# Kernel optimization log

Measured on AMD Instinct MI355X. Metric: run time of the kernel, lower is better.

Reference implementation:

```python
import jax, jax.numpy as jnp
import numpy as np

ALPHA = 0.5        # damping from conf['alpha']
MAX_ITERS = 30     # fixed-point iterations (conf uses up to 150 with eps early-exit)
GN_GROUPS = 3
GN_EPS = 1e-5
SLOPE = 0.01       # F.leaky_relu default negative_slope


def _conv(x, w, b, pad):
    y = jax.lax.conv_general_dilated(
        x, w, window_strides=(1, 1), padding=[(pad, pad), (pad, pad)],
        dimension_numbers=("NCHW", "OIHW", "NCHW"))
    return y + b[None, :, None, None]


def _leaky(x):
    return jnp.where(x >= 0, x, SLOPE * x)


def _groupnorm(x, gamma, beta):
    N, C, H, W = x.shape
    xg = x.reshape(N, GN_GROUPS, C // GN_GROUPS, H, W)
    mu = xg.mean(axis=(2, 3, 4), keepdims=True)
    var = xg.var(axis=(2, 3, 4), keepdims=True)
    xg = (xg - mu) * jax.lax.rsqrt(var + GN_EPS)
    x = xg.reshape(N, C, H, W)
    return x * gamma[None, :, None, None] + beta[None, :, None, None]


def setup_inputs() -> dict:
    key = jax.random.key(0)
    ks = jax.random.split(key, 8)
    image = jax.random.normal(ks[0], (1024, 3, 32, 32), dtype=jnp.float32)
    # Unit params (small init keeps the fixed-point iteration contractive)
    w1 = jax.random.normal(ks[1], (6, 8, 5, 5), dtype=jnp.float32) * 0.05
    b1 = jnp.zeros((6,), jnp.float32)
    gamma = jnp.ones((6,), jnp.float32)
    beta = jnp.zeros((6,), jnp.float32)
    w2 = jax.random.normal(ks[2], (5, 6, 5, 5), dtype=jnp.float32) * 0.05
    b2 = jnp.zeros((5,), jnp.float32)
    # detection head: Conv2d(5, 10, 32, padding=0) -> full-image conv
    wh = jax.random.normal(ks[3], (10, 5, 32, 32), dtype=jnp.float32) * 0.01
    bh = jnp.zeros((10,), jnp.float32)
    return {"image": image, "w1": w1, "b1": b1, "gamma": gamma, "beta": beta,
            "w2": w2, "b2": b2, "wh": wh, "bh": bh}


def reference(image, w1, b1, gamma, beta, w2, b2, wh, bh):
    N = image.shape[0]
    z0 = jnp.zeros((N, 5, 32, 32), image.dtype)

    def unit(z):
        zx = jnp.concatenate([z, image], axis=1)
        h = _groupnorm(_leaky(_conv(zx, w1, b1, 2)), gamma, beta)
        return _leaky(_conv(h, w2, b2, 2))

    def step(z, _):
        z = (1.0 - ALPHA) * z + ALPHA * unit(z)
        return z, None

    z, _ = jax.lax.scan(step, z0, None, length=MAX_ITERS)
    return _conv(z, wh, bh, 0)
```

## Files before the change

### kernel.cpp

```cpp
#include <hip/hip_runtime.h>
#include <hip/hip_fp16.h>


typedef _Float16 half8 __attribute__((ext_vector_type(8)));
typedef float f32x4 __attribute__((ext_vector_type(4)));

#define PLANE 5184
#define HB    5184
#define WL1   10368
#define WL2   12928
#define NLDS  15488

__device__ __forceinline__ unsigned pk2(float a, float b) {
    __half2 h = __float22half2_rn(make_float2(a, b));
    return *reinterpret_cast<unsigned*>(&h);
}
__device__ __forceinline__ float2 up2(unsigned u) {
    __half2 h = *reinterpret_cast<__half2*>(&u);
    return __half22float2(h);
}
__device__ __forceinline__ unsigned hmul2(unsigned a, unsigned b) {
    __half2 r = __hmul2(*reinterpret_cast<__half2*>(&a), *reinterpret_cast<__half2*>(&b));
    return *reinterpret_cast<unsigned*>(&r);
}
__device__ __forceinline__ float lrelu(float x) { return fmaxf(x, 0.01f * x); }
__device__ __forceinline__ int bofs(int y, int x) {
    return ((y * 36 + x) * 16) ^ ((x & 8) << 1);
}

__global__ void pack_weights(const float* __restrict__ w1,
                             const float* __restrict__ w2,
                             unsigned* __restrict__ ws)
{
    int t = blockIdx.x * 256 + threadIdx.x;
    if (t < 640) {
        int c = t >> 6, l = t & 63;
        int row = l & 15, tg = l >> 4;
        int dx = row >> 3, oc = row & 7;
        int ty = c >> 1, tx = 4 * (c & 1) + tg, kx = tx - dx;
        unsigned q[4];
        #pragma unroll
        for (int d = 0; d < 4; ++d) {
            float v0 = 0.f, v1 = 0.f;
            if (oc < 6 && kx >= 0 && kx < 5) {
                v0 = w1[(oc * 8 + 2 * d) * 25 + ty * 5 + kx];
                v1 = w1[(oc * 8 + 2 * d + 1) * 25 + ty * 5 + kx];
            }
            q[d] = pk2(v0, v1);
        }
        *(uint4*)&ws[t * 4] = make_uint4(q[0], q[1], q[2], q[3]);
    } else if (t < 1280) {
        int u = t - 640;
        int c = u >> 6, l = u & 63;
        int row = l & 15, tg = l >> 4;
        int dx = row >> 3, oc = row & 7;
        int ty = c >> 1, tx = 4 * (c & 1) + tg, kx = tx - dx;
        unsigned q[4];
        #pragma unroll
        for (int d = 0; d < 4; ++d) {
            float v0 = 0.f, v1 = 0.f;
            if (oc < 5 && kx >= 0 && kx < 5) {
                if (2 * d < 6)     v0 = w2[(oc * 6 + 2 * d) * 25 + ty * 5 + kx];
                if (2 * d + 1 < 6) v1 = w2[(oc * 6 + 2 * d + 1) * 25 + ty * 5 + kx];
            }
            q[d] = pk2(v0, v1);
        }
        *(uint4*)&ws[2560 + u * 4] = make_uint4(q[0], q[1], q[2], q[3]);
    } else if (t < 1310) {
        int idx = t - 1280;
        int oc = idx / 6, ch = idx % 6;
        float s = 0.f;
        for (int tap = 0; tap < 25; ++tap) s += w2[(oc * 6 + ch) * 25 + tap];
        ((float*)ws)[5120 + idx] = s;
    }
}

__global__ __launch_bounds__(256, 2)
void deq_kernel(const float* __restrict__ image,
                const unsigned* __restrict__ wks,
                const float* __restrict__ b1,
                const float* __restrict__ gam, const float* __restrict__ bet,
                const float* __restrict__ b2,
                const float* __restrict__ wh, const float* __restrict__ bh,
                float* __restrict__ out)
{
    __shared__ __align__(16) unsigned lds[NLDS];
    __shared__ float red[48];
    __shared__ float s2s[32];

    const int n    = blockIdx.x;
    const int tid  = threadIdx.x;
    const int lane = tid & 63;
    const int wid  = tid >> 6;
    const int col  = lane & 15;
    const int tg   = lane >> 4;
    const int dxl  = tg >> 1;
    const int sub  = tg & 1;

    for (int p = tid; p < 2 * PLANE; p += 256) lds[p] = 0u;
    for (int p = tid; p < 2560; p += 256) {
        lds[WL1 + p] = wks[p];
        lds[WL2 + p] = wks[2560 + p];
    }
    if (tid < 30) s2s[tid] = ((const float*)wks)[5120 + tid];
    __syncthreads();

    {
        const int yy = tid >> 3, xx0 = (tid & 7) << 2;
        float4 i0 = *(const float4*)&image[(n * 3 + 0) * 1024 + yy * 32 + xx0];
        float4 i1 = *(const float4*)&image[(n * 3 + 1) * 1024 + yy * 32 + xx0];
        float4 i2 = *(const float4*)&image[(n * 3 + 2) * 1024 + yy * 32 + xx0];
        float a0[4] = {i0.x, i0.y, i0.z, i0.w};
        float a1[4] = {i1.x, i1.y, i1.z, i1.w};
        float a2[4] = {i2.x, i2.y, i2.z, i2.w};
        #pragma unroll
        for (int i = 0; i < 4; ++i) {
            unsigned* bp = (unsigned*)((char*)lds + bofs(yy + 2, xx0 + 2 + i));
            bp[2] = pk2(0.f, a0[i]);
            bp[3] = pk2(a1[i], a2[i]);
        }
    }

    int sx2[2];
    #pragma unroll
    for (int txh = 0; txh < 2; ++txh) {
        int x = 2 * col + 4 * txh + tg;
        sx2[txh] = (x * 16) ^ ((x & 8) << 1);
    }

    float b1q[4], b2q[4];
    #pragma unroll
    for (int r = 0; r < 4; ++r) {
        int oc = (tg * 4 + r) & 7;
        b1q[r] = (oc < 6) ? b1[oc] : 0.f;
        b2q[r] = (oc < 5) ? b2[oc] : 0.f;
    }
    const f32x4 ai1 = {b1q[0], b1q[1], b1q[2], b1q[3]};

    __syncthreads();

    const char* zb  = (const char*)lds;
    const char* hbB = (const char*)lds + HB * 4;
    const int ay0 = wid << 3;
    const int wlo = lane << 2;

    #pragma unroll 1
    for (int it = 0; it < 30; ++it) {
        uint4 f1[10];
        #pragma unroll
        for (int c = 0; c < 10; ++c)
            f1[c] = *(const uint4*)&lds[WL1 + c * 256 + wlo];

        f32x4 acc[8];
        #pragma unroll
        for (int g = 0; g < 8; ++g) acc[g] = ai1;

        #pragma unroll
        for (int pr = 0; pr < 12; ++pr) {
            const char* rowp = zb + (ay0 + pr) * 576;
            #pragma unroll
            for (int txh = 0; txh < 2; ++txh) {
                half8 pv = *(const half8*)(rowp + sx2[txh]);
                #pragma unroll
                for (int ty = 0; ty < 5; ++ty) {
                    const int g = pr - ty;
                    if (g >= 0 && g < 8)
                        acc[g] = __builtin_amdgcn_mfma_f32_16x16x32_f16(
                            __builtin_bit_cast(half8, f1[ty * 2 + txh]), pv, acc[g], 0, 0, 0);
                }
            }
        }

        float ps_lo = 0.f, ps_hi = 0.f, pq_lo = 0.f, pq_hi = 0.f;
        #pragma unroll
        for (int g = 0; g < 8; ++g) {
            float h0 = lrelu(acc[g][0]), h1 = lrelu(acc[g][1]);
            float h2 = lrelu(acc[g][2]), h3 = lrelu(acc[g][3]);
            ps_lo += h0 + h1;  pq_lo = fmaf(h0, h0, fmaf(h1, h1, pq_lo));
            ps_hi += h2 + h3;  pq_hi = fmaf(h2, h2, fmaf(h3, h3, pq_hi));
            char* wp = (char*)lds + HB * 4 + bofs(ay0 + g + 2, 2 * col + dxl + 2) + sub * 8;
            *(uint2*)wp = make_uint2(pk2(h0, h1), pk2(h2, h3));
        }

        #pragma unroll
        for (int m = 1; m <= 8; m <<= 1) {
            ps_lo += __shfl_xor(ps_lo, m); ps_hi += __shfl_xor(ps_hi, m);
            pq_lo += __shfl_xor(pq_lo, m); pq_hi += __shfl_xor(pq_hi, m);
        }
        ps_lo += __shfl_xor(ps_lo, 32); ps_hi += __shfl_xor(ps_hi, 32);
        pq_lo += __shfl_xor(pq_lo, 32); pq_hi += __shfl_xor(pq_hi, 32);
        if (lane == 0)  { red[wid * 8 + 0] = ps_lo; red[wid * 8 + 1] = ps_hi;
                          red[wid * 8 + 4] = pq_lo; red[wid * 8 + 5] = pq_hi; }
        if (lane == 16) { red[wid * 8 + 2] = ps_lo; red[wid * 8 + 6] = pq_lo; }
        __syncthreads();

        float scv[6], shv[6];
        #pragma unroll
        for (int g3 = 0; g3 < 3; ++g3) {
            float s = 0.f, q = 0.f;
            #pragma unroll
            for (int w = 0; w < 4; ++w) { s += red[w * 8 + g3]; q += red[w * 8 + 4 + g3]; }
            float mean = s * (1.f / 2048.f);
            float var  = q * (1.f / 2048.f) - mean * mean;
            float inv  = rsqrtf(var + 1e-5f);
            #pragma unroll
            for (int k = 0; k < 2; ++k) {
                int c = 2 * g3 + k;
                scv[c] = inv * gam[c];
                shv[c] = bet[c] - mean * scv[c];
            }
        }
        f32x4 ai2;
        #pragma unroll
        for (int r = 0; r < 4; ++r) {
            int ocr = (tg * 4 + r) & 7;
            int base = (ocr < 5) ? ocr * 6 : 0;
            float db = 0.f;
            #pragma unroll
            for (int ch = 0; ch < 6; ++ch) db = fmaf(s2s[base + ch], shv[ch], db);
            ai2[r] = b2q[r] + ((ocr < 5) ? db : 0.f);
        }
        unsigned sp0 = pk2(scv[0], scv[1]), sp1 = pk2(scv[2], scv[3]), sp2 = pk2(scv[4], scv[5]);
        {
            float ph[6];
            #pragma unroll
            for (int c = 0; c < 6; ++c) {
                float rs = (fabsf(scv[c]) > 1e-20f) ? 1.f / scv[c] : 0.f;
                ph[c] = -shv[c] * rs;
            }
            uint4 padq = make_uint4(pk2(ph[0], ph[1]), pk2(ph[2], ph[3]), pk2(ph[4], ph[5]), 0u);
            for (int t = tid; t < 272; t += 256) {
                int row, cc;
                if (t < 72)       { row = t / 36;             cc = t % 36; }
                else if (t < 144) { row = 34 + (t - 72) / 36; cc = (t - 72) % 36; }
                else {
                    int q4 = t - 144;
                    row = 2 + (q4 >> 2);
                    int c4 = q4 & 3;
                    cc = (c4 < 2) ? c4 : c4 + 32;
                }
                *(uint4*)((char*)lds + HB * 4 + bofs(row, cc)) = padq;
            }
        }
        __syncthreads();

        uint4 f2[10];
        #pragma unroll
        for (int c = 0; c < 10; ++c) {
            uint4 wr = *(const uint4*)&lds[WL2 + c * 256 + wlo];
            f2[c].x = hmul2(wr.x, sp0);
            f2[c].y = hmul2(wr.y, sp1);
            f2[c].z = hmul2(wr.z, sp2);
            f2[c].w = 0u;
        }
        #pragma unroll
        for (int g = 0; g < 8; ++g) acc[g] = ai2;

        #pragma unroll
        for (int pr = 0; pr < 12; ++pr) {
            const char* rowp = hbB + (ay0 + pr) * 576;
            #pragma unroll
            for (int txh = 0; txh < 2; ++txh) {
                half8 pv = *(const half8*)(rowp + sx2[txh]);
                #pragma unroll
                for (int ty = 0; ty < 5; ++ty) {
                    const int g = pr - ty;
                    if (g >= 0 && g < 8)
                        acc[g] = __builtin_amdgcn_mfma_f32_16x16x32_f16(
                            __builtin_bit_cast(half8, f2[ty * 2 + txh]), pv, acc[g], 0, 0, 0);
                }
            }
        }

        #pragma unroll
        for (int g = 0; g < 8; ++g) {
            char* zp = (char*)lds + bofs(ay0 + g + 2, 2 * col + dxl + 2);
            if (sub == 0) {
                uint2 zo = *(uint2*)zp;
                float2 za = up2(zo.x), zc = up2(zo.y);
                float z0 = 0.5f * za.x + 0.5f * lrelu(acc[g][0]);
                float z1 = 0.5f * za.y + 0.5f * lrelu(acc[g][1]);
                float z2 = 0.5f * zc.x + 0.5f * lrelu(acc[g][2]);
                float z3 = 0.5f * zc.y + 0.5f * lrelu(acc[g][3]);
                *(uint2*)zp = make_uint2(pk2(z0, z1), pk2(z2, z3));
            } else {
                _Float16* pz = (_Float16*)(zp + 8);
                float z4 = 0.5f * (float)pz[0] + 0.5f * lrelu(acc[g][0]);
                pz[0] = (_Float16)z4;
            }
        }
        __syncthreads();
    }

    {
        const int yy = tid >> 3, xx0 = (tid & 7) << 2;
        float zf[5][4];
        #pragma unroll
        for (int i = 0; i < 4; ++i) {
            const unsigned* bp = (const unsigned*)((const char*)lds + bofs(yy + 2, xx0 + 2 + i));
            float2 f0 = up2(bp[0]), f1 = up2(bp[1]), f2 = up2(bp[2]);
            zf[0][i] = f0.x; zf[1][i] = f0.y; zf[2][i] = f1.x; zf[3][i] = f1.y; zf[4][i] = f2.x;
        }
        float ho[10];
        #pragma unroll
        for (int o = 0; o < 10; ++o) ho[o] = 0.f;
        #pragma unroll
        for (int c = 0; c < 5; ++c) {
            #pragma unroll
            for (int o = 0; o < 10; ++o) {
                float4 wv = *(const float4*)&wh[(o * 5 + c) * 1024 + yy * 32 + xx0];
                ho[o] = fmaf(zf[c][0], wv.x, ho[o]);
                ho[o] = fmaf(zf[c][1], wv.y, ho[o]);
                ho[o] = fmaf(zf[c][2], wv.z, ho[o]);
                ho[o] = fmaf(zf[c][3], wv.w, ho[o]);
            }
        }
        #pragma unroll
        for (int m = 1; m < 64; m <<= 1) {
            #pragma unroll
            for (int o = 0; o < 10; ++o) ho[o] += __shfl_xor(ho[o], m);
        }
        if (lane == 0) {
            #pragma unroll
            for (int o = 0; o < 10; ++o) red[wid * 10 + o] = ho[o];
        }
    }
    __syncthreads();
    if (tid < 10)
        out[n * 10 + tid] = red[tid] + red[10 + tid] + red[20 + tid] + red[30 + tid] + bh[tid];
}

extern "C" void kernel_launch(void* const* d_in, const int* in_sizes, int n_in,
                              void* d_out, int out_size, void* d_ws, size_t ws_size,
                              hipStream_t stream) {
    const float* image = (const float*)d_in[0];
    const float* w1    = (const float*)d_in[1];
    const float* b1    = (const float*)d_in[2];
    const float* gam   = (const float*)d_in[3];
    const float* bet   = (const float*)d_in[4];
    const float* w2    = (const float*)d_in[5];
    const float* b2    = (const float*)d_in[6];
    const float* wh    = (const float*)d_in[7];
    const float* bh    = (const float*)d_in[8];
    float* out = (float*)d_out;
    unsigned* ws = (unsigned*)d_ws;

    pack_weights<<<6, 256, 0, stream>>>(w1, w2, ws);

    const int N = in_sizes[0] / (3 * 32 * 32);
    deq_kernel<<<N, 256, 0, stream>>>(image, ws, b1, gam, bet, b2, wh, bh, out);
}
```

Baseline: 352.7 us.

## Apply GroupNorm explicitly and keep both conv weight sets in registers

Drops the trick of folding the GroupNorm scale into the per-iteration conv2 weights and its shift into a bias, which also needed special padding values written into the halo each iteration. The kernel now normalizes the activations directly before storing them to LDS, with a zero halo. Both weight fragment sets are loaded once into registers instead of being re-read from LDS every iteration, and the z and h planes share one LDS buffer. Launch bounds drop from 2 to 1 blocks per SIMD group, so register pressure rises and occupancy may fall.

New measurement: 309.6 us. 1.14x faster.

```diff
diff --git a/kernel.cpp b/kernel.cpp
--- a/kernel.cpp
+++ b/kernel.cpp
@@ -5,11 +5,8 @@
 typedef _Float16 half8 __attribute__((ext_vector_type(8)));
 typedef float f32x4 __attribute__((ext_vector_type(4)));
 
-#define PLANE 5184
-#define HB    5184
-#define WL1   10368
-#define WL2   12928
-#define NLDS  15488
+#define HOFF  34
+#define NBUF  (71 * 36 * 4)
 
 __device__ __forceinline__ unsigned pk2(float a, float b) {
     __half2 h = __float22half2_rn(make_float2(a, b));
@@ -19,13 +16,9 @@
     __half2 h = *reinterpret_cast<__half2*>(&u);
     return __half22float2(h);
 }
-__device__ __forceinline__ unsigned hmul2(unsigned a, unsigned b) {
-    __half2 r = __hmul2(*reinterpret_cast<__half2*>(&a), *reinterpret_cast<__half2*>(&b));
-    return *reinterpret_cast<unsigned*>(&r);
-}
 __device__ __forceinline__ float lrelu(float x) { return fmaxf(x, 0.01f * x); }
-__device__ __forceinline__ int bofs(int y, int x) {
-    return ((y * 36 + x) * 16) ^ ((x & 8) << 1);
+__device__ __forceinline__ int bofs(int r, int x) {
+    return ((r * 36 + x) * 16) ^ ((x & 8) << 1);
 }
 
 __global__ void pack_weights(const float* __restrict__ w1,
@@ -66,16 +59,10 @@
             q[d] = pk2(v0, v1);
         }
         *(uint4*)&ws[2560 + u * 4] = make_uint4(q[0], q[1], q[2], q[3]);
-    } else if (t < 1310) {
-        int idx = t - 1280;
-        int oc = idx / 6, ch = idx % 6;
-        float s = 0.f;
-        for (int tap = 0; tap < 25; ++tap) s += w2[(oc * 6 + ch) * 25 + tap];
-        ((float*)ws)[5120 + idx] = s;
-    }
-}
-
-__global__ __launch_bounds__(256, 2)
+    }
+}
+
+__global__ __launch_bounds__(256, 1)
 void deq_kernel(const float* __restrict__ image,
                 const unsigned* __restrict__ wks,
                 const float* __restrict__ b1,
@@ -84,9 +71,8 @@
                 const float* __restrict__ wh, const float* __restrict__ bh,
                 float* __restrict__ out)
 {
-    __shared__ __align__(16) unsigned lds[NLDS];
+    __shared__ __align__(16) unsigned buf[NBUF];
     __shared__ float red[48];
-    __shared__ float s2s[32];
 
     const int n    = blockIdx.x;
     const int tid  = threadIdx.x;
@@ -97,12 +83,7 @@
     const int dxl  = tg >> 1;
     const int sub  = tg & 1;
 
-    for (int p = tid; p < 2 * PLANE; p += 256) lds[p] = 0u;
-    for (int p = tid; p < 2560; p += 256) {
-        lds[WL1 + p] = wks[p];
-        lds[WL2 + p] = wks[2560 + p];
-    }
-    if (tid < 30) s2s[tid] = ((const float*)wks)[5120 + tid];
+    for (int p = tid; p < NBUF; p += 256) buf[p] = 0u;
     __syncthreads();
 
     {
@@ -115,10 +96,17 @@
         float a2[4] = {i2.x, i2.y, i2.z, i2.w};
         #pragma unroll
         for (int i = 0; i < 4; ++i) {
-            unsigned* bp = (unsigned*)((char*)lds + bofs(yy + 2, xx0 + 2 + i));
+            unsigned* bp = (unsigned*)((char*)buf + bofs(yy + 2, xx0 + 2 + i));
             bp[2] = pk2(0.f, a0[i]);
             bp[3] = pk2(a1[i], a2[i]);
         }
+    }
+
+    uint4 f1[10], f2[10];
+    #pragma unroll
+    for (int c = 0; c < 10; ++c) {
+        f1[c] = *(const uint4*)&wks[(c * 64 + lane) * 4];
+        f2[c] = *(const uint4*)&wks[2560 + (c * 64 + lane) * 4];
     }
 
     int sx2[2];
@@ -128,29 +116,27 @@
         sx2[txh] = (x * 16) ^ ((x & 8) << 1);
     }
 
-    float b1q[4], b2q[4];
+    const int chb = (tg & 1) * 4;
+    float b1q[4], b2q[4], gq[4], bq[4];
     #pragma unroll
     for (int r = 0; r < 4; ++r) {
-        int oc = (tg * 4 + r) & 7;
+        int oc = chb + r;
         b1q[r] = (oc < 6) ? b1[oc] : 0.f;
         b2q[r] = (oc < 5) ? b2[oc] : 0.f;
+        gq[r]  = (oc < 6) ? gam[oc] : 0.f;
+        bq[r]  = (oc < 6) ? bet[oc] : 0.f;
     }
     const f32x4 ai1 = {b1q[0], b1q[1], b1q[2], b1q[3]};
+    const f32x4 ai2 = {b2q[0], b2q[1], b2q[2], b2q[3]};
 
     __syncthreads();
 
-    const char* zb  = (const char*)lds;
-    const char* hbB = (const char*)lds + HB * 4;
+    const char* zb = (const char*)buf;
     const int ay0 = wid << 3;
-    const int wlo = lane << 2;
+    const int hwp0 = bofs(0, 2 * col + dxl + 2) + sub * 8;
 
     #pragma unroll 1
     for (int it = 0; it < 30; ++it) {
-        uint4 f1[10];
-        #pragma unroll
-        for (int c = 0; c < 10; ++c)
-            f1[c] = *(const uint4*)&lds[WL1 + c * 256 + wlo];
-
         f32x4 acc[8];
         #pragma unroll
         for (int g = 0; g < 8; ++g) acc[g] = ai1;
@@ -176,10 +162,9 @@
         for (int g = 0; g < 8; ++g) {
             float h0 = lrelu(acc[g][0]), h1 = lrelu(acc[g][1]);
             float h2 = lrelu(acc[g][2]), h3 = lrelu(acc[g][3]);
+            acc[g][0] = h0; acc[g][1] = h1; acc[g][2] = h2; acc[g][3] = h3;
             ps_lo += h0 + h1;  pq_lo = fmaf(h0, h0, fmaf(h1, h1, pq_lo));
             ps_hi += h2 + h3;  pq_hi = fmaf(h2, h2, fmaf(h3, h3, pq_hi));
-            char* wp = (char*)lds + HB * 4 + bofs(ay0 + g + 2, 2 * col + dxl + 2) + sub * 8;
-            *(uint2*)wp = make_uint2(pk2(h0, h1), pk2(h2, h3));
         }
 
         #pragma unroll
@@ -194,7 +179,7 @@
         if (lane == 16) { red[wid * 8 + 2] = ps_lo; red[wid * 8 + 6] = pq_lo; }
         __syncthreads();
 
-        float scv[6], shv[6];
+        float invm[3], meanm[3];
         #pragma unroll
         for (int g3 = 0; g3 < 3; ++g3) {
             float s = 0.f, q = 0.f;
@@ -202,63 +187,36 @@
             for (int w = 0; w < 4; ++w) { s += red[w * 8 + g3]; q += red[w * 8 + 4 + g3]; }
             float mean = s * (1.f / 2048.f);
             float var  = q * (1.f / 2048.f) - mean * mean;
-            float inv  = rsqrtf(var + 1e-5f);
-            #pragma unroll
-            for (int k = 0; k < 2; ++k) {
-                int c = 2 * g3 + k;
-                scv[c] = inv * gam[c];
-                shv[c] = bet[c] - mean * scv[c];
-            }
-        }
-        f32x4 ai2;
+            invm[g3]  = rsqrtf(var + 1e-5f);
+            meanm[g3] = mean;
+        }
+        float scq[4], shq[4];
         #pragma unroll
         for (int r = 0; r < 4; ++r) {
-            int ocr = (tg * 4 + r) & 7;
-            int base = (ocr < 5) ? ocr * 6 : 0;
-            float db = 0.f;
-            #pragma unroll
-            for (int ch = 0; ch < 6; ++ch) db = fmaf(s2s[base + ch], shv[ch], db);
-            ai2[r] = b2q[r] + ((ocr < 5) ? db : 0.f);
-        }
-        unsigned sp0 = pk2(scv[0], scv[1]), sp1 = pk2(scv[2], scv[3]), sp2 = pk2(scv[4], scv[5]);
-        {
-            float ph[6];
-            #pragma unroll
-            for (int c = 0; c < 6; ++c) {
-                float rs = (fabsf(scv[c]) > 1e-20f) ? 1.f / scv[c] : 0.f;
-                ph[c] = -shv[c] * rs;
-            }
-            uint4 padq = make_uint4(pk2(ph[0], ph[1]), pk2(ph[2], ph[3]), pk2(ph[4], ph[5]), 0u);
-            for (int t = tid; t < 272; t += 256) {
-                int row, cc;
-                if (t < 72)       { row = t / 36;             cc = t % 36; }
-                else if (t < 144) { row = 34 + (t - 72) / 36; cc = (t - 72) % 36; }
-                else {
-                    int q4 = t - 144;
-                    row = 2 + (q4 >> 2);
-                    int c4 = q4 & 3;
-                    cc = (c4 < 2) ? c4 : c4 + 32;
-                }
-                *(uint4*)((char*)lds + HB * 4 + bofs(row, cc)) = padq;
-            }
+            int oc = chb + r;
+            float inv  = (oc < 6) ? invm[oc >> 1]  : 0.f;
+            float mean = (oc < 6) ? meanm[oc >> 1] : 0.f;
+            scq[r] = inv * gq[r];
+            shq[r] = bq[r] - mean * scq[r];
+        }
+
+        #pragma unroll
+        for (int g = 0; g < 8; ++g) {
+            float h0 = fmaf(acc[g][0], scq[0], shq[0]);
+            float h1 = fmaf(acc[g][1], scq[1], shq[1]);
+            float h2 = fmaf(acc[g][2], scq[2], shq[2]);
+            float h3 = fmaf(acc[g][3], scq[3], shq[3]);
+            char* wp = (char*)buf + (ay0 + g + 2 + HOFF) * 576 + hwp0;
+            *(uint2*)wp = make_uint2(pk2(h0, h1), pk2(h2, h3));
         }
         __syncthreads();
 
-        uint4 f2[10];
-        #pragma unroll
-        for (int c = 0; c < 10; ++c) {
-            uint4 wr = *(const uint4*)&lds[WL2 + c * 256 + wlo];
-            f2[c].x = hmul2(wr.x, sp0);
-            f2[c].y = hmul2(wr.y, sp1);
-            f2[c].z = hmul2(wr.z, sp2);
-            f2[c].w = 0u;
-        }
         #pragma unroll
         for (int g = 0; g < 8; ++g) acc[g] = ai2;
 
         #pragma unroll
         for (int pr = 0; pr < 12; ++pr) {
-            const char* rowp = hbB + (ay0 + pr) * 576;
+            const char* rowp = zb + (HOFF + ay0 + pr) * 576;
             #pragma unroll
             for (int txh = 0; txh < 2; ++txh) {
                 half8 pv = *(const half8*)(rowp + sx2[txh]);
@@ -274,7 +232,7 @@
 
         #pragma unroll
         for (int g = 0; g < 8; ++g) {
-            char* zp = (char*)lds + bofs(ay0 + g + 2, 2 * col + dxl + 2);
+            char* zp = (char*)buf + bofs(ay0 + g + 2, 2 * col + dxl + 2);
             if (sub == 0) {
                 uint2 zo = *(uint2*)zp;
                 float2 za = up2(zo.x), zc = up2(zo.y);
@@ -297,9 +255,9 @@
         float zf[5][4];
         #pragma unroll
         for (int i = 0; i < 4; ++i) {
-            const unsigned* bp = (const unsigned*)((const char*)lds + bofs(yy + 2, xx0 + 2 + i));
-            float2 f0 = up2(bp[0]), f1 = up2(bp[1]), f2 = up2(bp[2]);
-            zf[0][i] = f0.x; zf[1][i] = f0.y; zf[2][i] = f1.x; zf[3][i] = f1.y; zf[4][i] = f2.x;
+            const unsigned* bp = (const unsigned*)((const char*)buf + bofs(yy + 2, xx0 + 2 + i));
+            float2 f0 = up2(bp[0]), fb = up2(bp[1]), fc = up2(bp[2]);
+            zf[0][i] = f0.x; zf[1][i] = f0.y; zf[2][i] = fb.x; zf[3][i] = fb.y; zf[4][i] = fc.x;
         }
         float ho[10];
         #pragma unroll
@@ -345,7 +303,7 @@
     float* out = (float*)d_out;
     unsigned* ws = (unsigned*)d_ws;
 
-    pack_weights<<<6, 256, 0, stream>>>(w1, w2, ws);
+    pack_weights<<<5, 256, 0, stream>>>(w1, w2, ws);
 
     const int N = in_sizes[0] / (3 * 32 * 32);
     deq_kernel<<<N, 256, 0, stream>>>(image, ws, b1, gam, bet, b2, wh, bh, out);
```

## Recompute halo rows per wave to drop mid-iteration block barrier

Applied to the files above, without the earlier changes.

Each wave now computes the first conv over 12 output rows, its own 8 plus 2 halo rows on each side, and writes them to a private per-wave LDS region. The second conv reads only that private region, so the block-wide __syncthreads between the two convs becomes a local lgkmcnt wait. The z plane gains extra padding rows and launch bounds drop to one block per CU to fit the larger LDS footprint. The cost is 50% more MFMA work in conv1 and lower occupancy, traded for less barrier stall.

After: 390.5 us. 1.11x slower.

```diff
diff --git a/kernel.cpp b/kernel.cpp
--- a/kernel.cpp
+++ b/kernel.cpp
@@ -5,11 +5,11 @@
 typedef _Float16 half8 __attribute__((ext_vector_type(8)));
 typedef float f32x4 __attribute__((ext_vector_type(4)));
 
-#define PLANE 5184
-#define HB    5184
-#define WL1   10368
-#define WL2   12928
-#define NLDS  15488
+#define REG_DW  5760
+#define GRD_DW  12672
+#define WL1_DW  12816
+#define WL2_DW  15376
+#define NLDS_DW 17936
 
 __device__ __forceinline__ unsigned pk2(float a, float b) {
     __half2 h = __float22half2_rn(make_float2(a, b));
@@ -24,9 +24,7 @@
     return *reinterpret_cast<unsigned*>(&r);
 }
 __device__ __forceinline__ float lrelu(float x) { return fmaxf(x, 0.01f * x); }
-__device__ __forceinline__ int bofs(int y, int x) {
-    return ((y * 36 + x) * 16) ^ ((x & 8) << 1);
-}
+__device__ __forceinline__ int swz(int x) { return (x * 16) ^ ((x & 8) << 1); }
 
 __global__ void pack_weights(const float* __restrict__ w1,
                              const float* __restrict__ w2,
@@ -75,7 +73,7 @@
     }
 }
 
-__global__ __launch_bounds__(256, 2)
+__global__ __launch_bounds__(256, 1)
 void deq_kernel(const float* __restrict__ image,
                 const unsigned* __restrict__ wks,
                 const float* __restrict__ b1,
@@ -84,7 +82,7 @@
                 const float* __restrict__ wh, const float* __restrict__ bh,
                 float* __restrict__ out)
 {
-    __shared__ __align__(16) unsigned lds[NLDS];
+    __shared__ __align__(16) unsigned lds[NLDS_DW];
     __shared__ float red[48];
     __shared__ float s2s[32];
 
@@ -97,10 +95,10 @@
     const int dxl  = tg >> 1;
     const int sub  = tg & 1;
 
-    for (int p = tid; p < 2 * PLANE; p += 256) lds[p] = 0u;
+    for (int p = tid; p < GRD_DW + 144; p += 256) lds[p] = 0u;
     for (int p = tid; p < 2560; p += 256) {
-        lds[WL1 + p] = wks[p];
-        lds[WL2 + p] = wks[2560 + p];
+        lds[WL1_DW + p] = wks[p];
+        lds[WL2_DW + p] = wks[2560 + p];
     }
     if (tid < 30) s2s[tid] = ((const float*)wks)[5120 + tid];
     __syncthreads();
@@ -115,7 +113,7 @@
         float a2[4] = {i2.x, i2.y, i2.z, i2.w};
         #pragma unroll
         for (int i = 0; i < 4; ++i) {
-            unsigned* bp = (unsigned*)((char*)lds + bofs(yy + 2, xx0 + 2 + i));
+            unsigned* bp = (unsigned*)((char*)lds + (yy + 4) * 576 + swz(xx0 + 2 + i));
             bp[2] = pk2(0.f, a0[i]);
             bp[3] = pk2(a1[i], a2[i]);
         }
@@ -123,10 +121,8 @@
 
     int sx2[2];
     #pragma unroll
-    for (int txh = 0; txh < 2; ++txh) {
-        int x = 2 * col + 4 * txh + tg;
-        sx2[txh] = (x * 16) ^ ((x & 8) << 1);
-    }
+    for (int txh = 0; txh < 2; ++txh)
+        sx2[txh] = swz(2 * col + 4 * txh + tg);
 
     float b1q[4], b2q[4];
     #pragma unroll
@@ -139,9 +135,9 @@
 
     __syncthreads();
 
-    const char* zb  = (const char*)lds;
-    const char* hbB = (const char*)lds + HB * 4;
+    char* const regb = (char*)lds + REG_DW * 4 + wid * 6912;
     const int ay0 = wid << 3;
+    const int hwp0 = swz(2 * col + dxl + 2) + sub * 8;
     const int wlo = lane << 2;
 
     #pragma unroll 1
@@ -149,37 +145,38 @@
         uint4 f1[10];
         #pragma unroll
         for (int c = 0; c < 10; ++c)
-            f1[c] = *(const uint4*)&lds[WL1 + c * 256 + wlo];
-
-        f32x4 acc[8];
-        #pragma unroll
-        for (int g = 0; g < 8; ++g) acc[g] = ai1;
-
-        #pragma unroll
-        for (int pr = 0; pr < 12; ++pr) {
-            const char* rowp = zb + (ay0 + pr) * 576;
+            f1[c] = *(const uint4*)&lds[WL1_DW + c * 256 + wlo];
+
+        f32x4 acc[12];
+        #pragma unroll
+        for (int j = 0; j < 12; ++j) acc[j] = ai1;
+
+        #pragma unroll
+        for (int u = 0; u < 16; ++u) {
+            const char* rowp = (const char*)lds + (ay0 + u) * 576;
             #pragma unroll
             for (int txh = 0; txh < 2; ++txh) {
                 half8 pv = *(const half8*)(rowp + sx2[txh]);
                 #pragma unroll
                 for (int ty = 0; ty < 5; ++ty) {
-                    const int g = pr - ty;
-                    if (g >= 0 && g < 8)
-                        acc[g] = __builtin_amdgcn_mfma_f32_16x16x32_f16(
-                            __builtin_bit_cast(half8, f1[ty * 2 + txh]), pv, acc[g], 0, 0, 0);
+                    const int j = u - ty;
+                    if (j >= 0 && j < 12)
+                        acc[j] = __builtin_amdgcn_mfma_f32_16x16x32_f16(
+                            __builtin_bit_cast(half8, f1[ty * 2 + txh]), pv, acc[j], 0, 0, 0);
                 }
             }
         }
 
         float ps_lo = 0.f, ps_hi = 0.f, pq_lo = 0.f, pq_hi = 0.f;
         #pragma unroll
-        for (int g = 0; g < 8; ++g) {
-            float h0 = lrelu(acc[g][0]), h1 = lrelu(acc[g][1]);
-            float h2 = lrelu(acc[g][2]), h3 = lrelu(acc[g][3]);
-            ps_lo += h0 + h1;  pq_lo = fmaf(h0, h0, fmaf(h1, h1, pq_lo));
-            ps_hi += h2 + h3;  pq_hi = fmaf(h2, h2, fmaf(h3, h3, pq_hi));
-            char* wp = (char*)lds + HB * 4 + bofs(ay0 + g + 2, 2 * col + dxl + 2) + sub * 8;
-            *(uint2*)wp = make_uint2(pk2(h0, h1), pk2(h2, h3));
+        for (int j = 0; j < 12; ++j) {
+            float h0 = lrelu(acc[j][0]), h1 = lrelu(acc[j][1]);
+            float h2 = lrelu(acc[j][2]), h3 = lrelu(acc[j][3]);
+            if (j >= 2 && j <= 9) {
+                ps_lo += h0 + h1;  pq_lo = fmaf(h0, h0, fmaf(h1, h1, pq_lo));
+                ps_hi += h2 + h3;  pq_hi = fmaf(h2, h2, fmaf(h3, h3, pq_hi));
+            }
+            *(uint2*)(regb + j * 576 + hwp0) = make_uint2(pk2(h0, h1), pk2(h2, h3));
         }
 
         #pragma unroll
@@ -221,6 +218,7 @@
             ai2[r] = b2q[r] + ((ocr < 5) ? db : 0.f);
         }
         unsigned sp0 = pk2(scv[0], scv[1]), sp1 = pk2(scv[2], scv[3]), sp2 = pk2(scv[4], scv[5]);
+
         {
             float ph[6];
             #pragma unroll
@@ -229,63 +227,67 @@
                 ph[c] = -shv[c] * rs;
             }
             uint4 padq = make_uint4(pk2(ph[0], ph[1]), pk2(ph[2], ph[3]), pk2(ph[4], ph[5]), 0u);
-            for (int t = tid; t < 272; t += 256) {
-                int row, cc;
-                if (t < 72)       { row = t / 36;             cc = t % 36; }
-                else if (t < 144) { row = 34 + (t - 72) / 36; cc = (t - 72) % 36; }
-                else {
-                    int q4 = t - 144;
-                    row = 2 + (q4 >> 2);
-                    int c4 = q4 & 3;
-                    cc = (c4 < 2) ? c4 : c4 + 32;
-                }
-                *(uint4*)((char*)lds + HB * 4 + bofs(row, cc)) = padq;
-            }
-        }
-        __syncthreads();
+            if (lane < 48) {
+                int rr = lane >> 2, c4 = lane & 3;
+                int cc = (c4 < 2) ? c4 : c4 + 32;
+                *(uint4*)(regb + rr * 576 + swz(cc)) = padq;
+            }
+            if (wid == 0) {
+                #pragma unroll 1
+                for (int k = lane; k < 72; k += 64)
+                    *(uint4*)(regb + (k / 36) * 576 + swz(k % 36)) = padq;
+            }
+            if (wid == 3) {
+                #pragma unroll 1
+                for (int k = lane; k < 72; k += 64)
+                    *(uint4*)(regb + (10 + k / 36) * 576 + swz(k % 36)) = padq;
+            }
+        }
+        asm volatile("s_waitcnt lgkmcnt(0)" ::: "memory");
 
         uint4 f2[10];
         #pragma unroll
         for (int c = 0; c < 10; ++c) {
-            uint4 wr = *(const uint4*)&lds[WL2 + c * 256 + wlo];
+            uint4 wr = *(const uint4*)&lds[WL2_DW + c * 256 + wlo];
             f2[c].x = hmul2(wr.x, sp0);
             f2[c].y = hmul2(wr.y, sp1);
             f2[c].z = hmul2(wr.z, sp2);
             f2[c].w = 0u;
         }
-        #pragma unroll
-        for (int g = 0; g < 8; ++g) acc[g] = ai2;
-
-        #pragma unroll
-        for (int pr = 0; pr < 12; ++pr) {
-            const char* rowp = hbB + (ay0 + pr) * 576;
+        f32x4 a2c[8];
+        #pragma unroll
+        for (int g = 0; g < 8; ++g) a2c[g] = ai2;
+
+        #pragma unroll
+        for (int rr = 0; rr < 12; ++rr) {
+            const char* rowp = regb + rr * 576;
             #pragma unroll
             for (int txh = 0; txh < 2; ++txh) {
                 half8 pv = *(const half8*)(rowp + sx2[txh]);
                 #pragma unroll
                 for (int ty = 0; ty < 5; ++ty) {
-                    const int g = pr - ty;
+                    const int g = rr - ty;
                     if (g >= 0 && g < 8)
-                        acc[g] = __builtin_amdgcn_mfma_f32_16x16x32_f16(
-                            __builtin_bit_cast(half8, f2[ty * 2 + txh]), pv, acc[g], 0, 0, 0);
+                        a2c[g] = __builtin_amdgcn_mfma_f32_16x16x32_f16(
+                            __builtin_bit_cast(half8, f2[ty * 2 + txh]), pv, a2c[g], 0, 0, 0);
                 }
             }
         }
 
         #pragma unroll
         for (int g = 0; g < 8; ++g) {
-            char* zp = (char*)lds + bofs(ay0 + g + 2, 2 * col + dxl + 2);
+            char* zp = (char*)lds + (ay0 + g + 4) * 576 + swz(2 * col + dxl + 2);
             if (sub == 0) {
                 uint2 zo = *(uint2*)zp;
                 float2 za = up2(zo.x), zc = up2(zo.y);
-                float z0 = 0.5f * za.x + 0.5f * lrelu(acc[g][0]);
-                float z1 = 0.5f * za.y + 0.5f * lrelu(acc[g][1]);
-                float z2 = 0.5f * zc.x + 0.5f * lrelu(acc[g][2]);
-                float z3 = 0.5f * zc.y + 0.5f * lrelu(acc[g][3]);
+                float z0 = 0.5f * za.x + 0.5f * lrelu(a2c[g][0]);
+                float z1 = 0.5f * za.y + 0.5f * lrelu(a2c[g][1]);
+                float z2 = 0.5f * zc.x + 0.5f * lrelu(a2c[g][2]);
+                float z3 = 0.5f * zc.y + 0.5f * lrelu(a2c[g][3]);
                 *(uint2*)zp = make_uint2(pk2(z0, z1), pk2(z2, z3));
             } else {
                 _Float16* pz = (_Float16*)(zp + 8);
-                float z4 = 0.5f * (float)pz[0] + 0.5f * lrelu(acc[g][0]);
+                float z4 = 0.5f * (float)pz[0] + 0.5f * lrelu(a2c[g][0]);
                 pz[0] = (_Float16)z4;
             }
         }
@@ -297,9 +299,9 @@
         float zf[5][4];
         #pragma unroll
         for (int i = 0; i < 4; ++i) {
-            const unsigned* bp = (const unsigned*)((const char*)lds + bofs(yy + 2, xx0 + 2 + i));
-            float2 f0 = up2(bp[0]), f1 = up2(bp[1]), f2 = up2(bp[2]);
-            zf[0][i] = f0.x; zf[1][i] = f0.y; zf[2][i] = f1.x; zf[3][i] = f1.y; zf[4][i] = f2.x;
+            const unsigned* bp = (const unsigned*)((const char*)lds + (yy + 4) * 576 + swz(xx0 + 2 + i));
+            float2 f0 = up2(bp[0]), fb = up2(bp[1]), fc = up2(bp[2]);
+            zf[0][i] = f0.x; zf[1][i] = f0.y; zf[2][i] = fb.x; zf[3][i] = fb.y; zf[4][i] = fc.x;
         }
         float ho[10];
         #pragma unroll
```
